# Performance work log

Hardware: AMD Instinct MI355X
Metric: run time of the kernel (lower is better)

## Reference

```python
import jax, jax.numpy as jnp
import numpy as np

K = 100
TEMPERATURE = 0.1


def setup_inputs() -> dict:
    key = jax.random.key(0)
    k1, k2 = jax.random.split(key)
    x = jax.random.normal(k1, (8, 128, 60, 60), dtype=jnp.float32)
    W = jax.random.normal(k2, (128, 2 * K), dtype=jnp.float32) * 0.02  # torch Linear(k*2, d_model).weight
    b = jnp.zeros((128,), dtype=jnp.float32)
    return {"x": x, "W": W, "b": b}


def reference(x, W, b):
    x0, x1 = jnp.split(x, 2, axis=0)
    n, c, h, w = x0.shape
    hw = h * w
    # n c h w -> n (h w) c
    f0 = jnp.transpose(x0.reshape(n, c, hw), (0, 2, 1))
    f1 = jnp.transpose(x1.reshape(n, c, hw), (0, 2, 1))
    # (f0/sqrt(c)) @ (f1/sqrt(c))^T / T  ==  f0 @ f1^T / (c*T)
    sm = jnp.einsum('nld,nsd->nls', f0, f1) / (c * TEMPERATURE)
    cm = (jax.nn.softmax(sm, axis=1) * jax.nn.softmax(sm, axis=2)).reshape(n, hw * hw)
    _, topi = jax.lax.top_k(cm, K)  # (n, K)
    qindex = topi // hw
    rindex = topi % hw
    coords0 = jnp.stack([qindex % w, qindex // w], axis=-1).astype(jnp.float32) / w  # (n, K, 2) as (x, y)
    coords1 = jnp.stack([rindex % w, rindex // w], axis=-1).astype(jnp.float32) / w
    # create_meshgrid(h, w, normalized=False): (1, h*w, 2) with (x, y), row-major
    gy, gx = jnp.meshgrid(jnp.arange(h), jnp.arange(w), indexing='ij')
    grid = jnp.stack([gx, gy], axis=-1).reshape(1, hw, 2).astype(jnp.float32) / w
    offsets0 = grid[:, :, None, :] - coords0[:, None, :, :]  # (n, hw, K, 2)
    offsets1 = grid[:, :, None, :] - coords1[:, None, :, :]
    emb0 = offsets0.reshape(n, hw, 2 * K) @ W.T + b  # (n, hw, d_model)
    emb1 = offsets1.reshape(n, hw, 2 * K) @ W.T + b
    f0 = f0 + emb0
    f1 = f1 + emb1
    f = jnp.concatenate([f0, f1], axis=0)  # (2n, hw, d)
    # n (h w) d -> n d h w
    return jnp.transpose(f, (0, 2, 1)).reshape(2 * n, c, h, w)
```

## Files before the change

### kernel.cpp

```cpp
#include <hip/hip_runtime.h>

#define HW 3600
#define PADR 3712
#define NF4 900
#define CAP 16384
#define KSEL 100
#define NT 58
typedef unsigned long long U64;

using short8   = __attribute__((ext_vector_type(8))) short;
using float4v  = __attribute__((ext_vector_type(4))) float;
using float16v = __attribute__((ext_vector_type(16))) float;

__device__ __forceinline__ unsigned monof(float f) {
    unsigned b = __float_as_uint(f);
    return (b & 0x80000000u) ? ~b : (b | 0x80000000u);
}
__device__ __forceinline__ float unmonof(unsigned m) {
    return __uint_as_float((m & 0x80000000u) ? (m ^ 0x80000000u) : ~m);
}
__device__ __forceinline__ unsigned short f2bf(float f) {
    unsigned b = __float_as_uint(f);
    return (unsigned short)((b + 0x7FFFu + ((b >> 16) & 1u)) >> 16);
}
__device__ __forceinline__ float bf2f(unsigned short h) {
    return __uint_as_float(((unsigned)h) << 16);
}
__device__ __forceinline__ void async16(const void* g, void* l) {
    __builtin_amdgcn_global_load_lds((const __attribute__((address_space(1))) void*)g,
                                     (__attribute__((address_space(3))) void*)l, 16, 0, 0);
}


__global__ __launch_bounds__(256) void conv_k(
    const float* __restrict__ x,
    unsigned short* __restrict__ hiT, unsigned short* __restrict__ loT,
    unsigned* __restrict__ zero_region)
{
    int b = blockIdx.z, l0 = blockIdx.x * 64, d0 = blockIdx.y * 64;
    __shared__ float t[64][65];
    int tid = threadIdx.x;
    if (blockIdx.y == 0 && blockIdx.z == 0) {
        int base = blockIdx.x * 512;
        for (int i = tid; i < 512; i += 256) {
            int g = base + i;
            if (g < 28808) zero_region[g] = 0u;
        }
    }
#pragma unroll
    for (int r = 0; r < 4; r++) {
        int idx = tid + 256 * r;
        int d = idx >> 4, lq = idx & 15;
        int l = l0 + lq * 4;
        const float* src = x + ((size_t)b * 128 + d0 + d) * HW;
        float4 v;
        if (l + 3 < HW) v = *(const float4*)(src + l);
        else {
            v.x = (l     < HW) ? src[l]     : 0.f;
            v.y = (l + 1 < HW) ? src[l + 1] : 0.f;
            v.z = (l + 2 < HW) ? src[l + 2] : 0.f;
            v.w = (l + 3 < HW) ? src[l + 3] : 0.f;
        }
        t[lq * 4 + 0][d] = v.x; t[lq * 4 + 1][d] = v.y;
        t[lq * 4 + 2][d] = v.z; t[lq * 4 + 3][d] = v.w;
    }
    __syncthreads();
    const int rblk = l0 >> 7;
#pragma unroll
    for (int r = 0; r < 2; r++) {
        int idx = tid + 256 * r;
        int l = idx & 63, dq = idx >> 6;
        unsigned hp[4], lp[4];
#pragma unroll
        for (int j = 0; j < 4; j++) {
            float f0 = t[l][dq * 8 + 2 * j], f1 = t[l][dq * 8 + 2 * j + 1];
            unsigned short h0 = f2bf(f0), h1 = f2bf(f1);
            unsigned short g0 = f2bf(f0 - bf2f(h0)), g1 = f2bf(f1 - bf2f(h1));
            hp[j] = (unsigned)h0 | ((unsigned)h1 << 16);
            lp[j] = (unsigned)g0 | ((unsigned)g1 << 16);
        }
        size_t o = ((size_t)(b * 29 + rblk) * 16 + (d0 >> 3) + dq) * 1024
                 + (size_t)((l0 + l) & 127) * 8;
        *(uint4*)(hiT + o) = make_uint4(hp[0], hp[1], hp[2], hp[3]);
        *(uint4*)(loT + o) = make_uint4(lp[0], lp[1], lp[2], lp[3]);
    }
}

__global__ __launch_bounds__(512) void gemm_mfma_k(
    const unsigned short* __restrict__ hiT, const unsigned short* __restrict__ loT,
    float* __restrict__ den_row, float* __restrict__ den_col,
    float* __restrict__ maxvt)
{
    const int batch = blockIdx.z, bx = blockIdx.x, by = blockIdx.y;
    __shared__ __align__(16) union SU {
        unsigned short st[4][4][128][8];
        float T[8448];
    } u;
    __shared__ float rsB[128];
    __shared__ float csB[128];
    __shared__ unsigned mxB[2][128];

    const int tid = threadIdx.x;
    const int lane = tid & 63, w = tid >> 6;
    const int l31 = lane & 31, h = lane >> 5;
    const int p = w >> 1, halfr = w & 1;
    const int rg = w >> 2, cg = w & 3;

    const unsigned NEGM = monof(-3.4e38f);
    if (tid < 128) { rsB[tid] = 0.f; csB[tid] = 0.f; }
    if (tid < 256) mxB[tid >> 7][tid & 127] = NEGM;

    const unsigned short* psrc = (p == 0) ? hiT : (p == 1) ? loT : (p == 2) ? hiT : loT;
    const int bsel = (p < 2) ? batch : batch + 4;
    const int rblk = (p < 2) ? by : bx;
    const size_t cbase = ((size_t)(bsel * 29 + rblk) * 16) * 1024;

    float16v acc[2];
    acc[0] = (float16v)(0.f);
    acc[1] = (float16v)(0.f);

    for (int k0 = 0; k0 < 128; k0 += 32) {
#pragma unroll
        for (int kb = 0; kb < 4; kb++) {
            const unsigned short* g = psrc + cbase + (size_t)((k0 >> 3) + kb) * 1024
                                    + (halfr << 9) + lane * 8;
            async16(g, &u.st[p][kb][halfr << 6][0]);
        }
        __syncthreads();
#pragma unroll
        for (int j = 0; j < 2; j++) {
            int kb = j * 2 + h;
            short8 ah[2], al[2], bh, bl;
            ah[0] = *(const short8*)&u.st[0][kb][rg * 64 + l31][0];
            ah[1] = *(const short8*)&u.st[0][kb][rg * 64 + 32 + l31][0];
            al[0] = *(const short8*)&u.st[1][kb][rg * 64 + l31][0];
            al[1] = *(const short8*)&u.st[1][kb][rg * 64 + 32 + l31][0];
            bh    = *(const short8*)&u.st[2][kb][cg * 32 + l31][0];
            bl    = *(const short8*)&u.st[3][kb][cg * 32 + l31][0];
#pragma unroll
            for (int mt = 0; mt < 2; mt++) {
                acc[mt] = __builtin_amdgcn_mfma_f32_32x32x16_bf16(ah[mt], bh, acc[mt], 0, 0, 0);
                acc[mt] = __builtin_amdgcn_mfma_f32_32x32x16_bf16(ah[mt], bl, acc[mt], 0, 0, 0);
                acc[mt] = __builtin_amdgcn_mfma_f32_32x32x16_bf16(al[mt], bh, acc[mt], 0, 0, 0);
            }
        }
        __syncthreads();
    }

    const float scale = 0.078125f;
    float* T = u.T + w * (32 * 33);
    const bool interior = (bx < 28) && (by < 28);
    const int col0 = bx * 128 + cg * 32 + l31;
    const bool cv = interior || (col0 < HW);
    float cs = 0.f;

#pragma unroll
    for (int mt = 0; mt < 2; mt++) {
#pragma unroll
        for (int reg = 0; reg < 16; reg++) {
            float v = acc[mt][reg] * scale;
            float e = cv ? __expf(v) : 0.f;
            int rloc = (reg & 3) + 8 * (reg >> 2) + 4 * h;
            bool rv = interior || (by * 128 + rg * 64 + mt * 32 + rloc < HW);
            if (rv) cs += e;
            T[rloc * 33 + l31] = e;
        }
        __asm__ __volatile__("s_waitcnt lgkmcnt(0)" ::: "memory");
        {
            float ps = 0.f;
#pragma unroll
            for (int i = 0; i < 16; i++) ps += T[l31 * 33 + h * 16 + i];
            ps += __shfl_xor(ps, 32);
            if (h == 0) atomicAdd(&rsB[rg * 64 + mt * 32 + l31], ps);
        }
        __asm__ __volatile__("s_waitcnt lgkmcnt(0)" ::: "memory");
#pragma unroll
        for (int reg = 0; reg < 16; reg++) {
            float v = acc[mt][reg] * scale;
            int rloc = (reg & 3) + 8 * (reg >> 2) + 4 * h;
            T[rloc * 33 + l31] = cv ? v : -3.4e38f;
        }
        __asm__ __volatile__("s_waitcnt lgkmcnt(0)" ::: "memory");
        {
            float pm = -3.4e38f;
#pragma unroll
            for (int i = 0; i < 16; i++) pm = fmaxf(pm, T[l31 * 33 + h * 16 + i]);
            pm = fmaxf(pm, __shfl_xor(pm, 32));
            if (h == 0) atomicMax(&mxB[cg >> 1][rg * 64 + mt * 32 + l31], monof(pm));
        }
        __asm__ __volatile__("s_waitcnt lgkmcnt(0)" ::: "memory");
    }
    cs += __shfl_xor(cs, 32);
    if (h == 0) atomicAdd(&csB[cg * 32 + l31], cs);
    __syncthreads();

    if (tid < 128) {
        int l = by * 128 + tid;
        if (l < HW) atomicAdd(&den_row[(size_t)batch * HW + l], rsB[tid]);
        int s = bx * 128 + tid;
        if (s < HW) atomicAdd(&den_col[(size_t)batch * HW + s], csB[tid]);
    }
    if (tid < 256) {
        int tile = tid >> 7, row = tid & 127;
        int l = by * 128 + row;
        if (l < HW)
            maxvt[((size_t)batch * NT + bx * 2 + tile) * PADR + l] =
                unmonof(mxB[tile][row]);
    }
}

__global__ __launch_bounds__(256) void stat_k(
    const float* __restrict__ den_row, const float* __restrict__ den_col,
    const float* __restrict__ maxvt, float* __restrict__ keylb)
{
    const int b = blockIdx.z, tid = threadIdx.x;
    __shared__ float lncS[HW];
    __shared__ float mlsS[NT];
    for (int i = tid; i < HW; i += 256)
        lncS[i] = __logf(den_col[(size_t)b * HW + i]);
    __syncthreads();
    if (tid < NT) {
        float mx = -3.4e38f;
        int s0 = tid * 64, s1 = s0 + 64; if (s1 > HW) s1 = HW;
        for (int s = s0; s < s1; s++) mx = fmaxf(mx, lncS[s]);
        mlsS[tid] = (s0 < HW) ? mx : 1e30f;
    }
    __syncthreads();
    int j = blockIdx.x * 240 + tid;
    if (tid < 240 && j < HW) {
        const float* mvb = maxvt + (size_t)b * NT * PADR;
        float b0 = -3.4e38f, b1_ = -3.4e38f;
#pragma unroll 4
        for (int tt = 0; tt < 58; tt += 2) {
            b0  = fmaxf(b0,  2.0f * mvb[(size_t)tt * PADR + j]       - mlsS[tt]);
            b1_ = fmaxf(b1_, 2.0f * mvb[(size_t)(tt + 1) * PADR + j] - mlsS[tt + 1]);
        }
        keylb[(size_t)b * HW + j] = fmaxf(b0, b1_) - __logf(den_row[(size_t)b * HW + j]);
    }
}

__global__ __launch_bounds__(256) void tau_k(
    const float* __restrict__ keylb, float* __restrict__ tau)
{
    const int b = blockIdx.z, tid = threadIdx.x;
    __shared__ unsigned keyS[HW];
    __shared__ unsigned hist[4096];
    __shared__ unsigned hpc[256];
    __shared__ int b1S, c1S, b2S, lcnt;
    __shared__ unsigned bestS;
    __shared__ unsigned list[1024];

    for (int i = tid; i < 4096; i += 256) hist[i] = 0u;
    if (tid == 0) { lcnt = 0; bestS = 0u; }
    __syncthreads();
    for (int i = tid; i < HW; i += 256) {
        unsigned k = monof(keylb[(size_t)b * HW + i]);
        keyS[i] = k;
        atomicAdd(&hist[k >> 20], 1u);
    }
    __syncthreads();
    { unsigned s = 0; for (int j = 0; j < 16; j++) s += hist[tid * 16 + j]; hpc[tid] = s; }
    __syncthreads();
    if (tid == 0) {
        unsigned cum = 0; int cs_ = 255;
        for (; cs_ > 0; cs_--) { if (cum + hpc[cs_] >= (unsigned)KSEL) break; cum += hpc[cs_]; }
        int bb = cs_ * 16 + 15;
        for (; bb > cs_ * 16; bb--) { if (cum + hist[bb] >= (unsigned)KSEL) break; cum += hist[bb]; }
        b1S = bb; c1S = (int)cum;
    }
    __syncthreads();
    int b1 = b1S;
    for (int i = tid; i < 4096; i += 256) hist[i] = 0u;
    __syncthreads();
    for (int i = tid; i < HW; i += 256) {
        unsigned k = keyS[i];
        if ((int)(k >> 20) == b1) atomicAdd(&hist[(k >> 8) & 4095], 1u);
    }
    __syncthreads();
    { unsigned s = 0; for (int j = 0; j < 16; j++) s += hist[tid * 16 + j]; hpc[tid] = s; }
    __syncthreads();
    if (tid == 0) {
        unsigned cum = (unsigned)c1S; int cs_ = 255;
        for (; cs_ > 0; cs_--) { if (cum + hpc[cs_] >= (unsigned)KSEL) break; cum += hpc[cs_]; }
        int bb = cs_ * 16 + 15;
        for (; bb > cs_ * 16; bb--) { if (cum + hist[bb] >= (unsigned)KSEL) break; cum += hist[bb]; }
        b2S = bb;
    }
    __syncthreads();
    int b2 = b2S;
    for (int i = tid; i < HW; i += 256) {
        unsigned k = keyS[i]; int hb = (int)(k >> 20);
        if (hb > b1 || (hb == b1 && (int)((k >> 8) & 4095) >= b2)) {
            int p = atomicAdd(&lcnt, 1);
            if (p < 1024) list[p] = k;
        }
    }
    __syncthreads();
    int L = lcnt; if (L > 1024) L = 1024;
    for (int i = tid; i < L; i += 256) {
        unsigned e = list[i]; int c = 0;
        for (int j = 0; j < L; j++) c += (list[j] >= e) ? 1 : 0;
        if (c >= KSEL) atomicMax(&bestS, e);
    }
    __syncthreads();
    if (tid == 0) tau[b] = unmonof(bestS) - 3e-4f;
}

__global__ __launch_bounds__(256) void recollect_k(
    const unsigned short* __restrict__ hiT, const unsigned short* __restrict__ loT,
    const float* __restrict__ den_row, const float* __restrict__ den_col,
    const float* __restrict__ maxvt, const float* __restrict__ tau,
    uint2* __restrict__ cand, int* __restrict__ cnt)
{
    const int t = blockIdx.x, batch = blockIdx.y;
    const int tid = threadIdx.x;
    __shared__ float lnrS[HW];
    __shared__ float lncS[64];
    __shared__ int prS[2048];
    __shared__ int pcS;
    __shared__ float mnlS;

    if (tid < 64) {
        int c = t * 64 + tid;
        float lc = (c < HW) ? __logf(den_col[(size_t)batch * HW + c]) : 1e30f;
        lncS[tid] = lc;
        float mn = lc;
#pragma unroll
        for (int off = 1; off < 64; off <<= 1) mn = fminf(mn, __shfl_xor(mn, off));
        if (tid == 0) mnlS = mn;
    }
    for (int r = tid; r < HW; r += 256)
        lnrS[r] = __logf(den_row[(size_t)batch * HW + r]);
    if (tid == 0) pcS = 0;
    __syncthreads();

    const float tv = tau[batch];
    const float tvm = tv - 3e-4f;
    const float mnl = mnlS;
    const float* mv = maxvt + ((size_t)batch * NT + t) * PADR;
    for (int r = tid; r < HW; r += 256) {
        float bnd = 2.0f * mv[r] - lnrS[r] - mnl;
        if (bnd >= tvm) {
            int p = atomicAdd(&pcS, 1);
            if (p < 2048) prS[p] = r;
        }
    }
    __syncthreads();
    int pc = pcS; if (pc > 2048) pc = 2048;
    if (pc == 0) return;

    const int lane = tid & 63, w = tid >> 6;
    const int m = lane & 15, q = lane >> 4;
    const float scale = 0.078125f;
    const size_t abase = (size_t)batch * PADR * 128;
    const size_t bbase = (size_t)(batch + 4) * PADR * 128;

    for (int g = w; g * 16 < pc; g += 4) {
        int pi = g * 16 + m;
        int rowv = (pi < pc) ? prS[pi] : HW;
        float ldrv = (pi < pc) ? lnrS[rowv] : 0.f;
        size_t arow = abase + ((size_t)(rowv >> 7) * 16) * 1024 + (size_t)(rowv & 127) * 8;

        float4v acc[4];
#pragma unroll
        for (int i = 0; i < 4; i++) acc[i] = (float4v){0.f, 0.f, 0.f, 0.f};
#pragma unroll
        for (int k0 = 0; k0 < 128; k0 += 32) {
            int kb = (k0 >> 3) + q;
            short8 ah = *(const short8*)(hiT + arow + (size_t)kb * 1024);
            short8 al = *(const short8*)(loT + arow + (size_t)kb * 1024);
#pragma unroll
            for (int nt = 0; nt < 4; nt++) {
                int c = t * 64 + nt * 16 + m;
                size_t brow = bbase + ((size_t)(c >> 7) * 16 + kb) * 1024 + (size_t)(c & 127) * 8;
                short8 bh = *(const short8*)(hiT + brow);
                short8 bl = *(const short8*)(loT + brow);
                acc[nt] = __builtin_amdgcn_mfma_f32_16x16x32_bf16(ah, bh, acc[nt], 0, 0, 0);
                acc[nt] = __builtin_amdgcn_mfma_f32_16x16x32_bf16(ah, bl, acc[nt], 0, 0, 0);
                acc[nt] = __builtin_amdgcn_mfma_f32_16x16x32_bf16(al, bh, acc[nt], 0, 0, 0);
            }
        }
#pragma unroll
        for (int nt = 0; nt < 4; nt++) {
            int c = t * 64 + nt * 16 + m;
            if (c >= HW) continue;
            float ldc = lncS[nt * 16 + m];
#pragma unroll
            for (int r = 0; r < 4; r++) {
                int ri = q * 4 + r;
                if (g * 16 + ri >= pc) continue;
                int rowo = __shfl(rowv, ri);
                float ldro = __shfl(ldrv, ri);
                float v = acc[nt][r] * scale;
                float tt2 = 2.0f * v - ldro - ldc;
                if (tt2 >= tv) {
                    int p = atomicAdd(&cnt[batch], 1);
                    if (p < CAP)
                        cand[(size_t)batch * CAP + p] =
                            make_uint2(monof(tt2), (unsigned)(rowo * HW + c));
                }
            }
        }
    }
}

__global__ __launch_bounds__(256) void final_k(
    const float* __restrict__ x, const float* __restrict__ W,
    const float* __restrict__ bias,
    const uint2* __restrict__ cand, const int* __restrict__ cnt,
    float* __restrict__ out)
{
    const int bd = blockIdx.x;
    const int b8 = bd >> 7, d = bd & 127;
    const int batch = b8 & 3;
    const bool useQ = (b8 < 4);
    const int tid = threadIdx.x;
    const int lane = tid & 63, w = tid >> 6;
    const uint2* cb = cand + (size_t)batch * CAP;

    __shared__ U64 lk[6144];
    __shared__ int topiS[KSEL];
    __shared__ float cxS[KSEL], cyS[KSEL];
    __shared__ float redC[4], redX[4], redY[4];
    __shared__ float cstS, sxS, syS;

    int M = cnt[batch]; if (M > CAP) M = CAP;
    const bool useL = (M <= 6144);
    if (useL)
        for (int i = tid; i < M; i += 256) {
            uint2 e = cb[i];
            lk[i] = ((U64)e.x << 32) | (unsigned)(~e.y);
        }
    __syncthreads();
    for (int i = tid; i < M; i += 256) {
        U64 e;
        if (useL) e = lk[i];
        else { uint2 tt = cb[i]; e = ((U64)tt.x << 32) | (unsigned)(~tt.y); }
        int r = 0;
        for (int j = 0; j < M; j++) {
            U64 o;
            if (useL) o = lk[j];
            else { uint2 tt = cb[j]; o = ((U64)tt.x << 32) | (unsigned)(~tt.y); }
            r += (o > e) ? 1 : 0;
        }
        if (r < KSEL) topiS[r] = (int)(~(unsigned)(e & 0xffffffffu));
    }
    __syncthreads();
    if (tid < KSEL) {
        int idx = topiS[tid];
        int qq = idx / HW, rr = idx - qq * HW;
        int sel = useQ ? qq : rr;
        cxS[tid] = (float)(sel % 60) / 60.0f;
        cyS[tid] = (float)(sel / 60) / 60.0f;
    }
    __syncthreads();
    float pC = 0.f, pX = 0.f, pY = 0.f;
    if (tid < KSEL) {
        float wx = W[d * 200 + 2 * tid], wy = W[d * 200 + 2 * tid + 1];
        pC = cxS[tid] * wx + cyS[tid] * wy;
        pX = wx; pY = wy;
    }
#pragma unroll
    for (int off = 1; off < 64; off <<= 1) {
        pC += __shfl_xor(pC, off);
        pX += __shfl_xor(pX, off);
        pY += __shfl_xor(pY, off);
    }
    if (lane == 0) { redC[w] = pC; redX[w] = pX; redY[w] = pY; }
    __syncthreads();
    if (tid == 0) {
        cstS = bias[d] - (redC[0] + redC[1] + redC[2] + redC[3]);
        sxS  = redX[0] + redX[1] + redX[2] + redX[3];
        syS  = redY[0] + redY[1] + redY[2] + redY[3];
    }
    __syncthreads();
    const float cst = cstS, sx = sxS, sy = syS;
    const float4* xin = (const float4*)(x + (size_t)bd * HW);
    float4* o4 = (float4*)(out + (size_t)bd * HW);
    for (int f = tid; f < NF4; f += 256) {
        float4 v = xin[f];
        int p0 = f * 4;
        float gy = (float)(p0 / 60) / 60.0f;
        float gxb = (float)(p0 % 60);
        float add = cst + gy * sy;
        v.x += add + ((gxb       ) / 60.0f) * sx;
        v.y += add + ((gxb + 1.f) / 60.0f) * sx;
        v.z += add + ((gxb + 2.f) / 60.0f) * sx;
        v.w += add + ((gxb + 3.f) / 60.0f) * sx;
        o4[f] = v;
    }
}

extern "C" void kernel_launch(void* const* d_in, const int* in_sizes, int n_in,
                              void* d_out, int out_size, void* d_ws, size_t ws_size,
                              hipStream_t stream)
{
    const float* x    = (const float*)d_in[0];
    const float* W    = (const float*)d_in[1];
    const float* bias = (const float*)d_in[2];
    float* out = (float*)d_out;

    char* ws = (char*)d_ws;
    float*    den_row = (float*)(ws + 0);
    float*    den_col = (float*)(ws + 57600);
    int*      cnt     = (int*)  (ws + 115200);
    float*    tau     = (float*)(ws + 115216);
    float*    keylb   = (float*)(ws + 115264);
    uint2*    cand    = (uint2*)(ws + 172864);
    float*    maxvt   = (float*)(ws + 697152);
    unsigned short* hiT = (unsigned short*)(ws + 4141888);
    unsigned short* loT = (unsigned short*)(ws + 11744064);

    conv_k     <<<dim3(58, 2, 8),  256, 0, stream>>>(x, hiT, loT, (unsigned*)ws);
    gemm_mfma_k<<<dim3(29, 29, 4), 512, 0, stream>>>(hiT, loT, den_row, den_col, maxvt);
    stat_k     <<<dim3(15, 1, 4),  256, 0, stream>>>(den_row, den_col, maxvt, keylb);
    tau_k      <<<dim3(1, 1, 4),   256, 0, stream>>>(keylb, tau);
    recollect_k<<<dim3(NT, 4),     256, 0, stream>>>(hiT, loT, den_row, den_col, maxvt, tau, cand, cnt);
    final_k    <<<dim3(1024),      256, 0, stream>>>(x, W, bias, cand, cnt, out);
}
```

Baseline: 221.1 us.

## Hoist top-k selection out of per-channel blocks and double-buffer GEMM staging

The top-k rank selection and the coordinate·W reductions move into a new select_k kernel that runs once per batch. Previously every one of the 1024 output blocks redid the quadratic candidate ranking. The GEMM now double-buffers its LDS tiles so async loads overlap the MFMAs. The epilogue fuses the row sum and row max into one pass, using a swizzled transpose buffer and taking the max as the log of the max exp. The max now depends on exp staying finite and adds one more kernel launch.

```diff
diff --git a/kernel.cpp b/kernel.cpp
--- a/kernel.cpp
+++ b/kernel.cpp
@@ -93,12 +93,15 @@
 {
     const int batch = blockIdx.z, bx = blockIdx.x, by = blockIdx.y;
     __shared__ __align__(16) union SU {
-        unsigned short st[4][4][128][8];
-        float T[8448];
+        unsigned short st[2][4][4][128][8];
+        struct {
+            float rs[128];
+            float cs[128];
+            unsigned mx[256];
+            float pad[7680];
+            float T[8192];
+        } ep;
     } u;
-    __shared__ float rsB[128];
-    __shared__ float csB[128];
-    __shared__ unsigned mxB[2][128];
 
     const int tid = threadIdx.x;
     const int lane = tid & 63, w = tid >> 6;
@@ -106,10 +109,6 @@
     const int p = w >> 1, halfr = w & 1;
     const int rg = w >> 2, cg = w & 3;
 
-    const unsigned NEGM = monof(-3.4e38f);
-    if (tid < 128) { rsB[tid] = 0.f; csB[tid] = 0.f; }
-    if (tid < 256) mxB[tid >> 7][tid & 127] = NEGM;
-
     const unsigned short* psrc = (p == 0) ? hiT : (p == 1) ? loT : (p == 2) ? hiT : loT;
     const int bsel = (p < 2) ? batch : batch + 4;
     const int rblk = (p < 2) ? by : bx;
@@ -119,24 +118,34 @@
     acc[0] = (float16v)(0.f);
     acc[1] = (float16v)(0.f);
 
-    for (int k0 = 0; k0 < 128; k0 += 32) {
-#pragma unroll
-        for (int kb = 0; kb < 4; kb++) {
-            const unsigned short* g = psrc + cbase + (size_t)((k0 >> 3) + kb) * 1024
-                                    + (halfr << 9) + lane * 8;
-            async16(g, &u.st[p][kb][halfr << 6][0]);
-        }
-        __syncthreads();
+#pragma unroll
+    for (int kb = 0; kb < 4; kb++) {
+        const unsigned short* g = psrc + cbase + (size_t)kb * 1024 + (halfr << 9) + lane * 8;
+        async16(g, &u.st[0][p][kb][halfr << 6][0]);
+    }
+    __syncthreads();
+
+#pragma unroll
+    for (int t = 0; t < 4; ++t) {
+        const int cur = t & 1;
+        if (t < 3) {
+#pragma unroll
+            for (int kb = 0; kb < 4; kb++) {
+                const unsigned short* g = psrc + cbase + (size_t)((t + 1) * 4 + kb) * 1024
+                                        + (halfr << 9) + lane * 8;
+                async16(g, &u.st[cur ^ 1][p][kb][halfr << 6][0]);
+            }
+        }
 #pragma unroll
         for (int j = 0; j < 2; j++) {
             int kb = j * 2 + h;
             short8 ah[2], al[2], bh, bl;
-            ah[0] = *(const short8*)&u.st[0][kb][rg * 64 + l31][0];
-            ah[1] = *(const short8*)&u.st[0][kb][rg * 64 + 32 + l31][0];
-            al[0] = *(const short8*)&u.st[1][kb][rg * 64 + l31][0];
-            al[1] = *(const short8*)&u.st[1][kb][rg * 64 + 32 + l31][0];
-            bh    = *(const short8*)&u.st[2][kb][cg * 32 + l31][0];
-            bl    = *(const short8*)&u.st[3][kb][cg * 32 + l31][0];
+            ah[0] = *(const short8*)&u.st[cur][0][kb][rg * 64 + l31][0];
+            ah[1] = *(const short8*)&u.st[cur][0][kb][rg * 64 + 32 + l31][0];
+            al[0] = *(const short8*)&u.st[cur][1][kb][rg * 64 + l31][0];
+            al[1] = *(const short8*)&u.st[cur][1][kb][rg * 64 + 32 + l31][0];
+            bh    = *(const short8*)&u.st[cur][2][kb][cg * 32 + l31][0];
+            bl    = *(const short8*)&u.st[cur][3][kb][cg * 32 + l31][0];
 #pragma unroll
             for (int mt = 0; mt < 2; mt++) {
                 acc[mt] = __builtin_amdgcn_mfma_f32_32x32x16_bf16(ah[mt], bh, acc[mt], 0, 0, 0);
@@ -147,8 +156,12 @@
         __syncthreads();
     }
 
+    if (tid < 128) { u.ep.rs[tid] = 0.f; u.ep.cs[tid] = 0.f; }
+    if (tid < 256) u.ep.mx[tid] = 0u;
+    __syncthreads();
+
     const float scale = 0.078125f;
-    float* T = u.T + w * (32 * 33);
+    float* T = u.ep.T + w * 1024;
     const bool interior = (bx < 28) && (by < 28);
     const int col0 = bx * 128 + cg * 32 + l31;
     const bool cv = interior || (col0 < HW);
@@ -163,49 +176,43 @@
             int rloc = (reg & 3) + 8 * (reg >> 2) + 4 * h;
             bool rv = interior || (by * 128 + rg * 64 + mt * 32 + rloc < HW);
             if (rv) cs += e;
-            T[rloc * 33 + l31] = e;
+            T[rloc * 32 + (l31 ^ rloc)] = e;
         }
         __asm__ __volatile__("s_waitcnt lgkmcnt(0)" ::: "memory");
         {
-            float ps = 0.f;
-#pragma unroll
-            for (int i = 0; i < 16; i++) ps += T[l31 * 33 + h * 16 + i];
+            float ps = 0.f, pm = 0.f;
+#pragma unroll
+            for (int i = 0; i < 16; i++) {
+                float tv_ = T[l31 * 32 + ((h * 16 + i) ^ l31)];
+                ps += tv_;
+                pm = fmaxf(pm, tv_);
+            }
             ps += __shfl_xor(ps, 32);
-            if (h == 0) atomicAdd(&rsB[rg * 64 + mt * 32 + l31], ps);
+            pm = fmaxf(pm, __shfl_xor(pm, 32));
+            if (h == 0) {
+                atomicAdd(&u.ep.rs[rg * 64 + mt * 32 + l31], ps);
+                atomicMax(&u.ep.mx[(cg >> 1) * 128 + rg * 64 + mt * 32 + l31],
+                          monof(__logf(pm)));
+            }
         }
         __asm__ __volatile__("s_waitcnt lgkmcnt(0)" ::: "memory");
-#pragma unroll
-        for (int reg = 0; reg < 16; reg++) {
-            float v = acc[mt][reg] * scale;
-            int rloc = (reg & 3) + 8 * (reg >> 2) + 4 * h;
-            T[rloc * 33 + l31] = cv ? v : -3.4e38f;
-        }
-        __asm__ __volatile__("s_waitcnt lgkmcnt(0)" ::: "memory");
-        {
-            float pm = -3.4e38f;
-#pragma unroll
-            for (int i = 0; i < 16; i++) pm = fmaxf(pm, T[l31 * 33 + h * 16 + i]);
-            pm = fmaxf(pm, __shfl_xor(pm, 32));
-            if (h == 0) atomicMax(&mxB[cg >> 1][rg * 64 + mt * 32 + l31], monof(pm));
-        }
-        __asm__ __volatile__("s_waitcnt lgkmcnt(0)" ::: "memory");
     }
     cs += __shfl_xor(cs, 32);
-    if (h == 0) atomicAdd(&csB[cg * 32 + l31], cs);
+    if (h == 0) atomicAdd(&u.ep.cs[cg * 32 + l31], cs);
     __syncthreads();
 
     if (tid < 128) {
         int l = by * 128 + tid;
-        if (l < HW) atomicAdd(&den_row[(size_t)batch * HW + l], rsB[tid]);
+        if (l < HW) atomicAdd(&den_row[(size_t)batch * HW + l], u.ep.rs[tid]);
         int s = bx * 128 + tid;
-        if (s < HW) atomicAdd(&den_col[(size_t)batch * HW + s], csB[tid]);
+        if (s < HW) atomicAdd(&den_col[(size_t)batch * HW + s], u.ep.cs[tid]);
     }
     if (tid < 256) {
         int tile = tid >> 7, row = tid & 127;
         int l = by * 128 + row;
         if (l < HW)
             maxvt[((size_t)batch * NT + bx * 2 + tile) * PADR + l] =
-                unmonof(mxB[tile][row]);
+                unmonof(u.ep.mx[tile * 128 + row]);
     }
 }
 
@@ -404,35 +411,27 @@
     }
 }
 
-__global__ __launch_bounds__(256) void final_k(
-    const float* __restrict__ x, const float* __restrict__ W,
-    const float* __restrict__ bias,
+__global__ __launch_bounds__(1024) void select_k(
     const uint2* __restrict__ cand, const int* __restrict__ cnt,
-    float* __restrict__ out)
-{
-    const int bd = blockIdx.x;
-    const int b8 = bd >> 7, d = bd & 127;
-    const int batch = b8 & 3;
-    const bool useQ = (b8 < 4);
+    const float* __restrict__ W, const float* __restrict__ bias,
+    float* __restrict__ cst, float* __restrict__ sxy)
+{
+    const int batch = blockIdx.x;
     const int tid = threadIdx.x;
-    const int lane = tid & 63, w = tid >> 6;
     const uint2* cb = cand + (size_t)batch * CAP;
-
     __shared__ U64 lk[6144];
     __shared__ int topiS[KSEL];
-    __shared__ float cxS[KSEL], cyS[KSEL];
-    __shared__ float redC[4], redX[4], redY[4];
-    __shared__ float cstS, sxS, syS;
+    __shared__ float cqx[KSEL], cqy[KSEL], crx[KSEL], cry[KSEL];
 
     int M = cnt[batch]; if (M > CAP) M = CAP;
     const bool useL = (M <= 6144);
     if (useL)
-        for (int i = tid; i < M; i += 256) {
+        for (int i = tid; i < M; i += 1024) {
             uint2 e = cb[i];
             lk[i] = ((U64)e.x << 32) | (unsigned)(~e.y);
         }
     __syncthreads();
-    for (int i = tid; i < M; i += 256) {
+    for (int i = tid; i < M; i += 1024) {
         U64 e;
         if (useL) e = lk[i];
         else { uint2 tt = cb[i]; e = ((U64)tt.x << 32) | (unsigned)(~tt.y); }
@@ -449,32 +448,38 @@
     if (tid < KSEL) {
         int idx = topiS[tid];
         int qq = idx / HW, rr = idx - qq * HW;
-        int sel = useQ ? qq : rr;
-        cxS[tid] = (float)(sel % 60) / 60.0f;
-        cyS[tid] = (float)(sel / 60) / 60.0f;
-    }
-    __syncthreads();
-    float pC = 0.f, pX = 0.f, pY = 0.f;
-    if (tid < KSEL) {
-        float wx = W[d * 200 + 2 * tid], wy = W[d * 200 + 2 * tid + 1];
-        pC = cxS[tid] * wx + cyS[tid] * wy;
-        pX = wx; pY = wy;
-    }
-#pragma unroll
-    for (int off = 1; off < 64; off <<= 1) {
-        pC += __shfl_xor(pC, off);
-        pX += __shfl_xor(pX, off);
-        pY += __shfl_xor(pY, off);
-    }
-    if (lane == 0) { redC[w] = pC; redX[w] = pX; redY[w] = pY; }
-    __syncthreads();
-    if (tid == 0) {
-        cstS = bias[d] - (redC[0] + redC[1] + redC[2] + redC[3]);
-        sxS  = redX[0] + redX[1] + redX[2] + redX[3];
-        syS  = redY[0] + redY[1] + redY[2] + redY[3];
-    }
-    __syncthreads();
-    const float cst = cstS, sx = sxS, sy = syS;
+        cqx[tid] = (float)(qq % 60) / 60.0f;
+        cqy[tid] = (float)(qq / 60) / 60.0f;
+        crx[tid] = (float)(rr % 60) / 60.0f;
+        cry[tid] = (float)(rr / 60) / 60.0f;
+    }
+    __syncthreads();
+    if (tid < 256) {
+        const int d = tid & 127, hf = tid >> 7;
+        const float* wrow = W + d * 200;
+        float sx = 0.f, sy = 0.f, c = 0.f;
+#pragma unroll 4
+        for (int k = 0; k < KSEL; k++) {
+            float wx = wrow[2 * k], wy = wrow[2 * k + 1];
+            sx += wx; sy += wy;
+            float cx = hf ? crx[k] : cqx[k];
+            float cy = hf ? cry[k] : cqy[k];
+            c += cx * wx + cy * wy;
+        }
+        cst[(hf ? (batch + 4) : batch) * 128 + d] = bias[d] - c;
+        if (batch == 0 && hf == 0) { sxy[d] = sx; sxy[128 + d] = sy; }
+    }
+}
+
+__global__ __launch_bounds__(256) void final_k(
+    const float* __restrict__ x, const float* __restrict__ cst,
+    const float* __restrict__ sxy, float* __restrict__ out)
+{
+    const int bd = blockIdx.x;
+    const int d = bd & 127;
+    const int tid = threadIdx.x;
+    const float cstv = cst[bd];
+    const float sx = sxy[d], sy = sxy[128 + d];
     const float4* xin = (const float4*)(x + (size_t)bd * HW);
     float4* o4 = (float4*)(out + (size_t)bd * HW);
     for (int f = tid; f < NF4; f += 256) {
@@ -482,8 +487,8 @@
         int p0 = f * 4;
         float gy = (float)(p0 / 60) / 60.0f;
         float gxb = (float)(p0 % 60);
-        float add = cst + gy * sy;
-        v.x += add + ((gxb       ) / 60.0f) * sx;
+        float add = cstv + gy * sy;
+        v.x += add + ((gxb      ) / 60.0f) * sx;
         v.y += add + ((gxb + 1.f) / 60.0f) * sx;
         v.z += add + ((gxb + 2.f) / 60.0f) * sx;
         v.w += add + ((gxb + 3.f) / 60.0f) * sx;
@@ -506,6 +511,8 @@
     int*      cnt     = (int*)  (ws + 115200);
     float*    tau     = (float*)(ws + 115216);
     float*    keylb   = (float*)(ws + 115264);
+    float*    cst     = (float*)(ws + 115264);
+    float*    sxy     = (float*)(ws + 119360);
     uint2*    cand    = (uint2*)(ws + 172864);
     float*    maxvt   = (float*)(ws + 697152);
     unsigned short* hiT = (unsigned short*)(ws + 4141888);
@@ -516,5 +523,6 @@
     stat_k     <<<dim3(15, 1, 4),  256, 0, stream>>>(den_row, den_col, maxvt, keylb);
     tau_k      <<<dim3(1, 1, 4),   256, 0, stream>>>(keylb, tau);
     recollect_k<<<dim3(NT, 4),     256, 0, stream>>>(hiT, loT, den_row, den_col, maxvt, tau, cand, cnt);
-    final_k    <<<dim3(1024),      256, 0, stream>>>(x, W, bias, cand, cnt, out);
-}
+    select_k   <<<dim3(4),         1024, 0, stream>>>(cand, cnt, W, bias, cst, sxy);
+    final_k    <<<dim3(1024),      256, 0, stream>>>(x, cst, sxy, out);
+}
```

After: 226.2 us. 1.02x slower.
